# Kernel optimization log

Hardware: AMD Instinct MI355X
Metric: run time of the kernel (lower is better)

## Reference

```python
import jax, jax.numpy as jnp
import numpy as np
from jax import lax


def _fps(xyz, num_group):
    """Farthest point sampling. xyz: (B, N, 3) -> centers (B, G, 3).
    Sequential over G (structural loop) via lax.scan; starts at index 0."""
    B, N, _ = xyz.shape

    def step(carry, _):
        min_d, last_idx = carry                      # (B, N), (B,)
        last_pt = jax.vmap(lambda p, i: p[i])(xyz, last_idx)  # (B, 3)
        d = jnp.sum((xyz - last_pt[:, None, :]) ** 2, axis=-1)  # (B, N)
        min_d = jnp.minimum(min_d, d)
        nxt = jnp.argmax(min_d, axis=-1).astype(jnp.int32)
        return (min_d, nxt), last_idx

    init = (jnp.full((B, N), jnp.inf, dtype=xyz.dtype),
            jnp.zeros((B,), dtype=jnp.int32))
    _, idxs = lax.scan(step, init, None, length=num_group)  # (G, B)
    idxs = idxs.T                                            # (B, G)
    centers = jax.vmap(lambda p, i: p[i])(xyz, idxs)         # (B, G, 3)
    return centers


def setup_inputs() -> dict:
    key = jax.random.key(0)
    xyz = jax.random.normal(key, (32, 8192, 3), dtype=jnp.float32)
    return {"xyz": xyz, "num_group": 256, "group_size": 32}


def reference(xyz, num_group, group_size):
    B, N, C = xyz.shape
    center = _fps(xyz, num_group)                            # (B, G, 3)
    # dense pairwise distances: (B, G, N)
    dist = jnp.linalg.norm(center[:, :, None, :] - xyz[:, None, :, :], axis=-1)
    _, idx = lax.top_k(-dist, group_size)                    # (B, G, k) smallest dists
    # gather neighbors per batch: (B, G, k, 3)
    patch = jax.vmap(lambda pts, i: pts[i])(xyz, idx)
    patch = patch - center[:, :, None, :]                    # recenter
    return (patch, center)
```

## Files before the change

kernel.cpp:

```cpp
#include <hip/hip_runtime.h>

#pragma clang fp contract(off)

#define BB 32
#define NN 8192
#define GG 256
#define KK 32

#define TFPS 512
#define JPF (NN / TFPS)

template <int CTRL>
__device__ __forceinline__ void rot_max(unsigned& hi, unsigned& lo) {
  const unsigned ohi =
      (unsigned)__builtin_amdgcn_update_dpp(0, (int)hi, CTRL, 0xF, 0xF, true);
  const unsigned olo =
      (unsigned)__builtin_amdgcn_update_dpp(0, (int)lo, CTRL, 0xF, 0xF, true);
  const bool gt = (ohi > hi) || ((ohi == hi) && (olo > lo));
  hi = gt ? ohi : hi;
  lo = gt ? olo : lo;
}

__global__ __launch_bounds__(TFPS, 1) void fps_kernel(const float* __restrict__ xyz,
                                                      float* __restrict__ out) {
#pragma clang fp contract(off)
  const int b = blockIdx.x;
  const int t = threadIdx.x;
  const int lane = t & 63;
  const int wave = t >> 6;
  const float* __restrict__ P = xyz + (size_t)b * NN * 3;

  __shared__ float4 pts[NN];
  __shared__ unsigned long long warr[2][32];

  float px[JPF], py[JPF], pz[JPF], md[JPF];
#pragma unroll
  for (int j = 0; j < JPF; ++j) {
    const int idx = t + j * TFPS;
    const float x = P[idx * 3 + 0];
    const float y = P[idx * 3 + 1];
    const float z = P[idx * 3 + 2];
    px[j] = x; py[j] = y; pz[j] = z;
    md[j] = __builtin_inff();
    pts[idx] = make_float4(x, y, z, 0.0f);
  }
  __syncthreads();

  unsigned win = 0;
  unsigned mywin = 0;

  for (int i = 0; i < GG; ++i) {
    if (t == i) mywin = win;
    if (i == GG - 1) break;

    const float4 c = pts[win];
    const float cx = c.x, cy = c.y, cz = c.z;

    float bv0 = -1.0f, bv1 = -1.0f;
    unsigned bi0 = 0, bi1 = 0;
#pragma unroll
    for (int j = 0; j < JPF; j += 2) {
      {
        const float dx = px[j] - cx;
        const float dy = py[j] - cy;
        const float dz = pz[j] - cz;
        const float d = dx * dx + dy * dy + dz * dz;
        const float m = md[j] < d ? md[j] : d;
        md[j] = m;
        if (m > bv0) { bv0 = m; bi0 = (unsigned)(t + j * TFPS); }
      }
      {
        const int jj = j + 1;
        const float dx = px[jj] - cx;
        const float dy = py[jj] - cy;
        const float dz = pz[jj] - cz;
        const float d = dx * dx + dy * dy + dz * dz;
        const float m = md[jj] < d ? md[jj] : d;
        md[jj] = m;
        if (m > bv1) { bv1 = m; bi1 = (unsigned)(t + jj * TFPS); }
      }
    }
    if (bv1 > bv0 || (bv1 == bv0 && bi1 < bi0)) { bv0 = bv1; bi0 = bi1; }

    unsigned hi = __float_as_uint(bv0);
    unsigned lo = ~bi0;
    rot_max<0x121>(hi, lo);
    rot_max<0x122>(hi, lo);
    rot_max<0x124>(hi, lo);
    rot_max<0x128>(hi, lo);

    if ((lane & 15) == 0)
      warr[i & 1][wave * 4 + (lane >> 4)] =
          ((unsigned long long)hi << 32) | lo;
    __syncthreads();

    const int g = lane & 15;
    const unsigned long long kA = warr[i & 1][g];
    const unsigned long long kB = warr[i & 1][g + 16];
    const unsigned long long k = kB > kA ? kB : kA;
    hi = (unsigned)(k >> 32);
    lo = (unsigned)k;
    rot_max<0x121>(hi, lo);
    rot_max<0x122>(hi, lo);
    rot_max<0x124>(hi, lo);
    rot_max<0x128>(hi, lo);

    win = ~lo;
  }

  if (t < GG) {
    const float4 c = pts[mywin];
    float* __restrict__ co =
        out + (size_t)BB * GG * KK * 3 + ((size_t)b * GG + t) * 3;
    co[0] = c.x; co[1] = c.y; co[2] = c.z;
  }
}

__global__ __launch_bounds__(512, 1) void knn_kernel(const float* __restrict__ xyz,
                                                     float* __restrict__ out) {
#pragma clang fp contract(off)
  const int b = blockIdx.x >> 3;
  const int chunk = blockIdx.x & 7;
  const int t = threadIdx.x;
  const int lane = t & 63;
  const int wave = t >> 6;
  const float* __restrict__ P = xyz + (size_t)b * NN * 3;

  __shared__ float xs[NN], ys[NN], zs[NN];
  __shared__ unsigned long long cand[8][256];

  for (int pt = t; pt < NN; pt += 512) {
    xs[pt] = P[pt * 3 + 0];
    ys[pt] = P[pt * 3 + 1];
    zs[pt] = P[pt * 3 + 2];
  }
  __syncthreads();

  const float* __restrict__ cent = out + (size_t)BB * GG * KK * 3;

  for (int gi = 0; gi < 4; ++gi) {
    const int g = chunk * 32 + wave * 4 + gi;
    const float cx = cent[((size_t)b * GG + g) * 3 + 0];
    const float cy = cent[((size_t)b * GG + g) * 3 + 1];
    const float cz = cent[((size_t)b * GG + g) * 3 + 2];

    float d2r[128];
    float mn = __builtin_inff();
#pragma unroll
    for (int j = 0; j < 128; ++j) {
      const int idx = lane + j * 64;
      const float dx = xs[idx] - cx;
      const float dy = ys[idx] - cy;
      const float dz = zs[idx] - cz;
      const float d2 = dx * dx + dy * dy + dz * dz;
      d2r[j] = d2;
      mn = fminf(mn, d2);
    }

    float sm = mn;
#pragma unroll
    for (int k = 2; k <= 64; k <<= 1) {
#pragma unroll
      for (int j2 = k >> 1; j2 > 0; j2 >>= 1) {
        const float o = __shfl_xor(sm, j2, 64);
        const bool keepMin = (((lane & k) == 0) == ((lane & j2) == 0));
        sm = keepMin ? fminf(sm, o) : fmaxf(sm, o);
      }
    }
    const float v = __shfl(sm, 31, 64);
    const float vi = __uint_as_float(__float_as_uint(v) + 8);

    unsigned cnt = 0;
    unsigned long long* __restrict__ cb = cand[wave];
#pragma unroll
    for (int j = 0; j < 128; ++j) {
      const bool p = d2r[j] <= vi;
      const unsigned long long mk = __ballot(p);
      if (p) {
        const unsigned off = cnt + (unsigned)__popcll(mk & ((1ull << lane) - 1));
        if (off < 256)
          cb[off] = ((unsigned long long)__float_as_uint(d2r[j]) << 32) |
                    (unsigned)(lane + j * 64);
      }
      cnt += (unsigned)__popcll(mk);
    }
    if (cnt > 256) cnt = 256;

    auto conv = [](unsigned long long e) -> unsigned long long {
      const float d = sqrtf(__uint_as_float((unsigned)(e >> 32)));
      return ((unsigned long long)__float_as_uint(d) << 32) | (e & 0xFFFFFFFFull);
    };

    unsigned long long myk;
    if (cnt <= 64) {
      unsigned long long key = ~0ull;
      if ((unsigned)lane < cnt) key = conv(cb[lane]);
#pragma unroll
      for (int k = 2; k <= 64; k <<= 1) {
#pragma unroll
        for (int j2 = k >> 1; j2 > 0; j2 >>= 1) {
          const unsigned long long o = __shfl_xor(key, j2, 64);
          const bool keepMin = (((lane & k) == 0) == ((lane & j2) == 0));
          const unsigned long long lo = o < key ? o : key;
          const unsigned long long hi = o < key ? key : o;
          key = keepMin ? lo : hi;
        }
      }
      myk = key;
    } else {
      unsigned long long k0 = ~0ull, k1 = ~0ull, k2 = ~0ull, k3 = ~0ull;
      if ((unsigned)lane < cnt)         k0 = conv(cb[lane]);
      if ((unsigned)(lane + 64) < cnt)  k1 = conv(cb[lane + 64]);
      if ((unsigned)(lane + 128) < cnt) k2 = conv(cb[lane + 128]);
      if ((unsigned)(lane + 192) < cnt) k3 = conv(cb[lane + 192]);
      unsigned long long got = ~0ull;
      for (int r = 0; r < 32; ++r) {
        unsigned long long m01 = k0 < k1 ? k0 : k1;
        unsigned long long m23 = k2 < k3 ? k2 : k3;
        unsigned long long m = m01 < m23 ? m01 : m23;
#pragma unroll
        for (int s = 32; s > 0; s >>= 1) {
          const unsigned long long o = __shfl_xor(m, s, 64);
          m = o < m ? o : m;
        }
        if (lane == r) got = m;
        if (k0 == m) k0 = ~0ull;
        else if (k1 == m) k1 = ~0ull;
        else if (k2 == m) k2 = ~0ull;
        else if (k3 == m) k3 = ~0ull;
      }
      myk = got;
    }

    if (lane < KK) {
      const unsigned idx = (unsigned)(myk & 0xFFFFFFFFull);
      const float ox = xs[idx] - cx;
      const float oy = ys[idx] - cy;
      const float oz = zs[idx] - cz;
      float* __restrict__ po = out + ((size_t)(((size_t)b * GG + g) * KK + lane)) * 3;
      po[0] = ox; po[1] = oy; po[2] = oz;
    }
  }
}

extern "C" void kernel_launch(void* const* d_in, const int* in_sizes, int n_in,
                              void* d_out, int out_size, void* d_ws, size_t ws_size,
                              hipStream_t stream) {
  const float* xyz = (const float*)d_in[0];
  float* out = (float*)d_out;
  fps_kernel<<<dim3(BB), dim3(TFPS), 0, stream>>>(xyz, out);
  knn_kernel<<<dim3(BB * 8), dim3(512), 0, stream>>>(xyz, out);
}
```

Baseline: 362.3 us.

## Double FPS block to 1024 threads and pack KNN xy in swizzled float2 LDS

The FPS kernel now uses 1024 threads per batch, so each thread holds 8 points instead of 16. The per-thread argmax collapses to a single chain, and the cross-wave reduction now reads 64 wave/group keys instead of 32. This shortens the serial per-iteration compute in the latency-bound FPS loop, at the cost of more register pressure limits and a wider block-level reduction. Separately, the KNN kernel stores x and y as swizzled float2 in LDS, cutting the number of LDS loads per point while trying to avoid bank conflicts.

```diff
diff --git a/kernel.cpp b/kernel.cpp
--- a/kernel.cpp
+++ b/kernel.cpp
@@ -7,7 +7,7 @@
 #define GG 256
 #define KK 32
 
-#define TFPS 512
+#define TFPS 1024
 #define JPF (NN / TFPS)
 
 template <int CTRL>
@@ -21,8 +21,8 @@
   lo = gt ? olo : lo;
 }
 
-__global__ __launch_bounds__(TFPS, 1) void fps_kernel(const float* __restrict__ xyz,
-                                                      float* __restrict__ out) {
+__global__ __launch_bounds__(TFPS) void fps_kernel(const float* __restrict__ xyz,
+                                                   float* __restrict__ out) {
 #pragma clang fp contract(off)
   const int b = blockIdx.x;
   const int t = threadIdx.x;
@@ -31,7 +31,7 @@
   const float* __restrict__ P = xyz + (size_t)b * NN * 3;
 
   __shared__ float4 pts[NN];
-  __shared__ unsigned long long warr[2][32];
+  __shared__ unsigned long long warr[2][64];
 
   float px[JPF], py[JPF], pz[JPF], md[JPF];
 #pragma unroll
@@ -56,34 +56,22 @@
     const float4 c = pts[win];
     const float cx = c.x, cy = c.y, cz = c.z;
 
-    float bv0 = -1.0f, bv1 = -1.0f;
-    unsigned bi0 = 0, bi1 = 0;
-#pragma unroll
-    for (int j = 0; j < JPF; j += 2) {
-      {
-        const float dx = px[j] - cx;
-        const float dy = py[j] - cy;
-        const float dz = pz[j] - cz;
-        const float d = dx * dx + dy * dy + dz * dz;
-        const float m = md[j] < d ? md[j] : d;
-        md[j] = m;
-        if (m > bv0) { bv0 = m; bi0 = (unsigned)(t + j * TFPS); }
-      }
-      {
-        const int jj = j + 1;
-        const float dx = px[jj] - cx;
-        const float dy = py[jj] - cy;
-        const float dz = pz[jj] - cz;
-        const float d = dx * dx + dy * dy + dz * dz;
-        const float m = md[jj] < d ? md[jj] : d;
-        md[jj] = m;
-        if (m > bv1) { bv1 = m; bi1 = (unsigned)(t + jj * TFPS); }
-      }
-    }
-    if (bv1 > bv0 || (bv1 == bv0 && bi1 < bi0)) { bv0 = bv1; bi0 = bi1; }
-
-    unsigned hi = __float_as_uint(bv0);
-    unsigned lo = ~bi0;
+    float bv = -1.0f;
+    int bj = 0;
+#pragma unroll
+    for (int j = 0; j < JPF; ++j) {
+      const float dx = px[j] - cx;
+      const float dy = py[j] - cy;
+      const float dz = pz[j] - cz;
+      const float d = dx * dx + dy * dy + dz * dz;
+      const float m = md[j] < d ? md[j] : d;
+      md[j] = m;
+      if (m > bv) { bv = m; bj = j; }
+    }
+    const unsigned bi = (unsigned)t + ((unsigned)bj << 10);
+
+    unsigned hi = __float_as_uint(bv);
+    unsigned lo = ~bi;
     rot_max<0x121>(hi, lo);
     rot_max<0x122>(hi, lo);
     rot_max<0x124>(hi, lo);
@@ -94,10 +82,15 @@
           ((unsigned long long)hi << 32) | lo;
     __syncthreads();
 
+    const unsigned long long* __restrict__ w = warr[i & 1];
     const int g = lane & 15;
-    const unsigned long long kA = warr[i & 1][g];
-    const unsigned long long kB = warr[i & 1][g + 16];
-    const unsigned long long k = kB > kA ? kB : kA;
+    const unsigned long long e0 = w[g];
+    const unsigned long long e1 = w[g + 16];
+    const unsigned long long e2 = w[g + 32];
+    const unsigned long long e3 = w[g + 48];
+    const unsigned long long ea = e0 > e1 ? e0 : e1;
+    const unsigned long long eb = e2 > e3 ? e2 : e3;
+    const unsigned long long k = ea > eb ? ea : eb;
     hi = (unsigned)(k >> 32);
     lo = (unsigned)k;
     rot_max<0x121>(hi, lo);
@@ -114,6 +107,10 @@
         out + (size_t)BB * GG * KK * 3 + ((size_t)b * GG + t) * 3;
     co[0] = c.x; co[1] = c.y; co[2] = c.z;
   }
+}
+
+__device__ __forceinline__ int swz(int idx) {
+  return idx ^ (((idx >> 4) & 3) << 2);
 }
 
 __global__ __launch_bounds__(512, 1) void knn_kernel(const float* __restrict__ xyz,
@@ -126,13 +123,13 @@
   const int wave = t >> 6;
   const float* __restrict__ P = xyz + (size_t)b * NN * 3;
 
-  __shared__ float xs[NN], ys[NN], zs[NN];
+  __shared__ float2 sxy[NN];
+  __shared__ float  sz[NN];
   __shared__ unsigned long long cand[8][256];
 
   for (int pt = t; pt < NN; pt += 512) {
-    xs[pt] = P[pt * 3 + 0];
-    ys[pt] = P[pt * 3 + 1];
-    zs[pt] = P[pt * 3 + 2];
+    sxy[swz(pt)] = make_float2(P[pt * 3 + 0], P[pt * 3 + 1]);
+    sz[pt] = P[pt * 3 + 2];
   }
   __syncthreads();
 
@@ -149,9 +146,11 @@
 #pragma unroll
     for (int j = 0; j < 128; ++j) {
       const int idx = lane + j * 64;
-      const float dx = xs[idx] - cx;
-      const float dy = ys[idx] - cy;
-      const float dz = zs[idx] - cz;
+      const float2 xy = sxy[swz(idx)];
+      const float zz = sz[idx];
+      const float dx = xy.x - cx;
+      const float dy = xy.y - cy;
+      const float dz = zz - cz;
       const float d2 = dx * dx + dy * dy + dz * dz;
       d2r[j] = d2;
       mn = fminf(mn, d2);
@@ -234,9 +233,11 @@
 
     if (lane < KK) {
       const unsigned idx = (unsigned)(myk & 0xFFFFFFFFull);
-      const float ox = xs[idx] - cx;
-      const float oy = ys[idx] - cy;
-      const float oz = zs[idx] - cz;
+      const float2 xy = sxy[swz((int)idx)];
+      const float zz = sz[idx];
+      const float ox = xy.x - cx;
+      const float oy = xy.y - cy;
+      const float oz = zz - cz;
       float* __restrict__ po = out + ((size_t)(((size_t)b * GG + g) * KK + lane)) * 3;
       po[0] = ox; po[1] = oy; po[2] = oz;
     }
```

Result: slower. 565.3 us (+56.0%).
